# Performance work log

Hardware: AMD Instinct MI355X
Metric: run time of the kernel (lower is better)

## Reference

```python
import jax, jax.numpy as jnp
import numpy as np

B, S, D, H = 8, 2048, 1024, 64  # batch, seq, dimension, attention_head_size


def setup_inputs() -> dict:
    key = jax.random.key(0)
    k0, k1, k2, k3 = jax.random.split(key, 4)
    scale = 1.0 / np.sqrt(D)  # keep activations sane
    return {
        "x": jax.random.normal(k0, (B, S, D), dtype=jnp.float32),
        "Wq": jax.random.normal(k1, (D, H), dtype=jnp.float32) * scale,
        "Wk": jax.random.normal(k2, (D, H), dtype=jnp.float32) * scale,
        "Wv": jax.random.normal(k3, (D, H), dtype=jnp.float32) * scale,
    }


def reference(x, Wq, Wk, Wv):
    # Linear projections (bias=False); W stored as [D, H] == torch weight.T
    q = jnp.einsum("bsd,dh->bsh", x, Wq)
    k = jnp.einsum("bsd,dh->bsh", x, Wk)
    v = jnp.einsum("bsd,dh->bsh", x, Wv)
    # full score matrix, scaled by sqrt(head_size)
    scores = jnp.einsum("bqh,bkh->bqk", q, k) / jnp.sqrt(jnp.float32(H))
    weights = jax.nn.softmax(scores, axis=-1)  # [B, S, S]
    # dropout p=0.0 (eval): identity
    out = jnp.einsum("bqk,bkh->bqh", weights, v)  # [B, S, H]
    return out, weights
```

## Files before the change

### kernel.cpp

```cpp
#include <hip/hip_runtime.h>

#define SB 8
#define SS 2048
#define SD 1024
#define SH 64

typedef float f32x4 __attribute__((ext_vector_type(4)));
typedef __bf16 bf16x8 __attribute__((ext_vector_type(8)));

__device__ __forceinline__ unsigned short f2bf(float f) {
  union { float f; unsigned int u; } v; v.f = f;
  unsigned int u = v.u;
  unsigned int r = u + 0x7FFFu + ((u >> 16) & 1u);
  return (unsigned short)(r >> 16);
}

__global__ void prep_wt(const float* __restrict__ Wq, const float* __restrict__ Wk,
                        const float* __restrict__ Wv, unsigned short* __restrict__ Wt) {
  int idx = blockIdx.x * 256 + threadIdx.x;
  int hc = idx >> 10, d = idx & 1023;
  const float* W = (hc < 64) ? Wq : (hc < 128) ? Wk : Wv;
  int h = hc & 63;
  Wt[idx] = f2bf(W[d * SH + h]);
}

__global__ void __launch_bounds__(512, 2) proj(
    const float* __restrict__ x, const unsigned short* __restrict__ Wt,
    unsigned short* __restrict__ Q, unsigned short* __restrict__ K,
    unsigned short* __restrict__ Vt) {
  __shared__ unsigned short xs[2][32 * 64];
  __shared__ unsigned short Bl[2][192 * 64];

  int tid = threadIdx.x;
  int w = tid >> 6, lane = tid & 63;
  int l15 = lane & 15, kg = lane >> 4;
  int wr = w >> 2, wc = w & 3;
  int m0 = blockIdx.x * 32;

  int srow = tid >> 4, sseg = tid & 15;
  const float* xp = x + (size_t)(m0 + srow) * SD + sseg * 4;
  int swoff = srow * 64 + (((sseg >> 1) ^ (srow & 7)) << 3) + ((sseg & 1) << 2);

#define STAGEB(tt, buf)                                                          \
  {                                                                              \
    _Pragma("unroll") for (int j = 0; j < 3; ++j) {                              \
      int Lb = w * 1024 + j * 8192 + lane * 16;                                  \
      int c = Lb >> 7, cb = Lb & 127;                                            \
      const char* srcp = (const char*)Wt + (size_t)c * 2048 + (tt) * 128 +       \
                         (cb ^ ((c & 7) << 4));                                  \
      __builtin_amdgcn_global_load_lds(                                          \
          (const __attribute__((address_space(1))) unsigned int*)(const void*)srcp, \
          (__attribute__((address_space(3))) unsigned int*)(void*)                \
              ((char*)&Bl[(buf)][0] + w * 1024 + j * 8192),                      \
          16, 0, 0);                                                             \
    }                                                                            \
  }

#define CVTW(RA, buf)                                                           \
  {                                                                             \
    ushort4 cv;                                                                 \
    cv.x = f2bf((RA).x); cv.y = f2bf((RA).y);                                   \
    cv.z = f2bf((RA).z); cv.w = f2bf((RA).w);                                   \
    *(ushort4*)(&xs[(buf)][0] + swoff) = cv;                                    \
  }

  f32x4 acc[3];
#pragma unroll
  for (int nt = 0; nt < 3; ++nt) acc[nt] = f32x4{0.f, 0.f, 0.f, 0.f};

  float4 ra = *(const float4*)xp;
  STAGEB(0, 0);
  CVTW(ra, 0);
  ra = *(const float4*)(xp + 64);
  __syncthreads();

  for (int t = 0; t < 16; ++t) {
    int cur = t & 1, nxt = (t + 1) & 1;
    if (t < 15) CVTW(ra, nxt);
    if (t < 14) ra = *(const float4*)(xp + (t + 2) * 64);
    if (t < 15) STAGEB(t + 1, nxt);

    const char* Bb = (const char*)&Bl[cur][0];
#pragma unroll
    for (int ks = 0; ks < 2; ++ks) {
      int row = wr * 16 + l15;
      int cg = ks * 4 + kg;
      bf16x8 af = *(const bf16x8*)(&xs[cur][0] + row * 64 + ((cg ^ (row & 7)) << 3));
#pragma unroll
      for (int nt = 0; nt < 3; ++nt) {
        int c = wc * 48 + nt * 16 + l15;
        int kb = (ks * 32 + kg * 8) * 2;
        bf16x8 bfr = *(const bf16x8*)(Bb + c * 128 + (kb ^ ((c & 7) << 4)));
        acc[nt] = __builtin_amdgcn_mfma_f32_16x16x32_bf16(af, bfr, acc[nt], 0, 0, 0);
      }
    }
    __syncthreads();
  }

#pragma unroll
  for (int nt = 0; nt < 3; ++nt) {
    int c = wc * 48 + nt * 16 + l15;
    int mat = c >> 6, h = c & 63;
#pragma unroll
    for (int r = 0; r < 4; ++r) {
      int row = m0 + wr * 16 + kg * 4 + r;
      unsigned short bv = f2bf(acc[nt][r]);
      if (mat == 0) {
        Q[(size_t)row * SH + h] = bv;
      } else if (mat == 1) {
        K[(size_t)row * SH + h] = bv;
      } else {
        int bb = row >> 11, key = row & 2047;
        Vt[((size_t)bb * SH + h) * SS + key] = bv;
      }
    }
  }
}

__global__ void __launch_bounds__(512, 4) attn(
    const unsigned short* __restrict__ Q, const unsigned short* __restrict__ Kb,
    const unsigned short* __restrict__ Vt, float* __restrict__ out,
    float* __restrict__ wts) {
  __shared__ float pf[8][16][68];
  __shared__ float mS[8][16], sgS[8][16];

  int b = blockIdx.x & 7, rg = blockIdx.x >> 3;
  int w = threadIdx.x >> 6, lane = threadIdx.x & 63;
  int l15 = lane & 15, kg = lane >> 4;
  int q0 = rg * 16;
  int kv0 = w * 256;

  const unsigned short* Qb  = Q  + (size_t)b * SS * SH;
  const unsigned short* Kbb = Kb + (size_t)b * SS * SH;
  const unsigned short* Vtb = Vt + (size_t)b * SH * SS;

  bf16x8 qf[2];
#pragma unroll
  for (int ks = 0; ks < 2; ++ks)
    qf[ks] = *(const bf16x8*)(Qb + (size_t)(q0 + l15) * SH + ks * 32 + kg * 8);

  f32x4 s[4][4];
#pragma unroll
  for (int kt = 0; kt < 4; ++kt)
#pragma unroll
    for (int n = 0; n < 4; ++n) s[kt][n] = f32x4{0.f, 0.f, 0.f, 0.f};

  for (int kt = 0; kt < 4; ++kt) {
#pragma unroll
    for (int ks = 0; ks < 2; ++ks)
#pragma unroll
      for (int n = 0; n < 4; ++n) {
        bf16x8 kf = *(const bf16x8*)(Kbb + (size_t)(kv0 + kt * 64 + n * 16 + l15) * SH + ks * 32 + kg * 8);
        s[kt][n] = __builtin_amdgcn_mfma_f32_16x16x32_bf16(qf[ks], kf, s[kt][n], 0, 0, 0);
      }
  }

  float m[4], sg[4];
#pragma unroll
  for (int r = 0; r < 4; ++r) {
    float mloc = -1e30f;
#pragma unroll
    for (int kt = 0; kt < 4; ++kt)
#pragma unroll
      for (int n = 0; n < 4; ++n) mloc = fmaxf(mloc, s[kt][n][r]);
    mloc *= 0.125f;
#pragma unroll
    for (int off = 1; off < 16; off <<= 1) mloc = fmaxf(mloc, __shfl_xor(mloc, off));
    float ssum = 0.f;
#pragma unroll
    for (int kt = 0; kt < 4; ++kt)
#pragma unroll
      for (int n = 0; n < 4; ++n) {
        float e = __expf(s[kt][n][r] * 0.125f - mloc);
        s[kt][n][r] = e;
        ssum += e;
      }
#pragma unroll
    for (int off = 1; off < 16; off <<= 1) ssum += __shfl_xor(ssum, off);
    m[r] = mloc; sg[r] = ssum;
  }

  if (l15 == 0) {
#pragma unroll
    for (int r = 0; r < 4; ++r) {
      mS[w][kg * 4 + r] = m[r];
      sgS[w][kg * 4 + r] = sg[r];
    }
  }
  __syncthreads();

  float scal[4];
#pragma unroll
  for (int r = 0; r < 4; ++r) {
    int row = kg * 4 + r;
    float M = -1e30f;
#pragma unroll
    for (int ww = 0; ww < 8; ++ww) M = fmaxf(M, mS[ww][row]);
    float Sg = 0.f;
#pragma unroll
    for (int ww = 0; ww < 8; ++ww) Sg += sgS[ww][row] * __expf(mS[ww][row] - M);
    scal[r] = __expf(m[r] - M) / Sg;
  }

  float* wb = wts + (size_t)b * SS * SS;
  f32x4 oacc[4];
#pragma unroll
  for (int nh = 0; nh < 4; ++nh) oacc[nh] = f32x4{0.f, 0.f, 0.f, 0.f};

  for (int kt = 0; kt < 4; ++kt) {
#pragma unroll
    for (int n = 0; n < 4; ++n)
#pragma unroll
      for (int r = 0; r < 4; ++r)
        pf[w][kg * 4 + r][n * 16 + l15] = s[kt][n][r] * scal[r];
    asm volatile("s_waitcnt lgkmcnt(0)" ::: "memory");

#pragma unroll
    for (int i = 0; i < 4; ++i) {
      int row = i * 4 + kg;
      f32x4 pv4 = *(const f32x4*)&pf[w][row][l15 * 4];
      *(f32x4*)(wb + (size_t)(q0 + row) * SS + kv0 + kt * 64 + l15 * 4) = pv4;
    }

#pragma unroll
    for (int ks = 0; ks < 2; ++ks) {
      f32x4 pa = *(const f32x4*)&pf[w][l15][ks * 32 + kg * 8];
      f32x4 pb = *(const f32x4*)&pf[w][l15][ks * 32 + kg * 8 + 4];
      union { unsigned short us[8]; bf16x8 v; } pu;
#pragma unroll
      for (int i = 0; i < 4; ++i) { pu.us[i] = f2bf(pa[i]); pu.us[4 + i] = f2bf(pb[i]); }
#pragma unroll
      for (int nh = 0; nh < 4; ++nh) {
        bf16x8 vf = *(const bf16x8*)(Vtb + (size_t)(nh * 16 + l15) * SS + kv0 + kt * 64 + ks * 32 + kg * 8);
        oacc[nh] = __builtin_amdgcn_mfma_f32_16x16x32_bf16(pu.v, vf, oacc[nh], 0, 0, 0);
      }
    }
  }

#pragma unroll
  for (int nh = 0; nh < 4; ++nh)
#pragma unroll
    for (int r = 0; r < 4; ++r)
      pf[w][kg * 4 + r][nh * 16 + l15] = oacc[nh][r];
  __syncthreads();

  int tid = threadIdx.x;
#pragma unroll
  for (int half = 0; half < 2; ++half) {
    int e = tid + half * 512;
    int row = e >> 6, col = e & 63;
    float ssum = 0.f;
#pragma unroll
    for (int ww = 0; ww < 8; ++ww) ssum += pf[ww][row][col];
    out[((size_t)b * SS + q0 + row) * SH + col] = ssum;
  }
}

extern "C" void kernel_launch(void* const* d_in, const int* in_sizes, int n_in,
                              void* d_out, int out_size, void* d_ws, size_t ws_size,
                              hipStream_t stream) {
  const float* x  = (const float*)d_in[0];
  const float* Wq = (const float*)d_in[1];
  const float* Wk = (const float*)d_in[2];
  const float* Wv = (const float*)d_in[3];

  unsigned short* Wt = (unsigned short*)d_ws;
  unsigned short* Q  = Wt + 192 * 1024;
  unsigned short* K  = Q + 16384 * 64;
  unsigned short* Vt = K + 16384 * 64;

  float* out = (float*)d_out;
  float* wts = out + (size_t)SB * SS * SH;

  prep_wt<<<768, 256, 0, stream>>>(Wq, Wk, Wv, Wt);
  proj<<<512, 512, 0, stream>>>(x, Wt, Q, K, Vt);
  attn<<<1024, 512, 0, stream>>>(Q, K, Vt, out, wts);
}
```

Before: 93.01 us.

## Split attention into QK-softmax kernel and separate weights-times-V kernel

Removes the P·V product from the attention kernel, which now only computes scores, softmax and writes the weight matrix. A new kernel reads the fp32 weights back from global memory together with transposed V, converts them to bf16 and accumulates the output with MFMA. It uses inline-asm global loads in a three-stage software pipeline. This frees registers and LDS work in the first kernel but adds a full re-read of the large weight matrix and an extra launch.

```diff
diff --git a/kernel.cpp b/kernel.cpp
--- a/kernel.cpp
+++ b/kernel.cpp
@@ -13,6 +13,10 @@
   unsigned int u = v.u;
   unsigned int r = u + 0x7FFFu + ((u >> 16) & 1u);
   return (unsigned short)(r >> 16);
+}
+
+__device__ __forceinline__ bf16x8 asbf(f32x4 x) {
+  union { f32x4 f; bf16x8 b; } u; u.f = x; return u.b;
 }
 
 __global__ void prep_wt(const float* __restrict__ Wq, const float* __restrict__ Wk,
@@ -117,9 +121,8 @@
   }
 }
 
-__global__ void __launch_bounds__(512, 4) attn(
+__global__ void __launch_bounds__(512, 4) qk_sm(
     const unsigned short* __restrict__ Q, const unsigned short* __restrict__ Kb,
-    const unsigned short* __restrict__ Vt, float* __restrict__ out,
     float* __restrict__ wts) {
   __shared__ float pf[8][16][68];
   __shared__ float mS[8][16], sgS[8][16];
@@ -132,7 +135,6 @@
 
   const unsigned short* Qb  = Q  + (size_t)b * SS * SH;
   const unsigned short* Kbb = Kb + (size_t)b * SS * SH;
-  const unsigned short* Vtb = Vt + (size_t)b * SH * SS;
 
   bf16x8 qf[2];
 #pragma unroll
@@ -203,10 +205,6 @@
   }
 
   float* wb = wts + (size_t)b * SS * SS;
-  f32x4 oacc[4];
-#pragma unroll
-  for (int nh = 0; nh < 4; ++nh) oacc[nh] = f32x4{0.f, 0.f, 0.f, 0.f};
-
   for (int kt = 0; kt < 4; ++kt) {
 #pragma unroll
     for (int n = 0; n < 4; ++n)
@@ -221,27 +219,71 @@
       f32x4 pv4 = *(const f32x4*)&pf[w][row][l15 * 4];
       *(f32x4*)(wb + (size_t)(q0 + row) * SS + kv0 + kt * 64 + l15 * 4) = pv4;
     }
-
-#pragma unroll
-    for (int ks = 0; ks < 2; ++ks) {
-      f32x4 pa = *(const f32x4*)&pf[w][l15][ks * 32 + kg * 8];
-      f32x4 pb = *(const f32x4*)&pf[w][l15][ks * 32 + kg * 8 + 4];
-      union { unsigned short us[8]; bf16x8 v; } pu;
-#pragma unroll
-      for (int i = 0; i < 4; ++i) { pu.us[i] = f2bf(pa[i]); pu.us[4 + i] = f2bf(pb[i]); }
-#pragma unroll
-      for (int nh = 0; nh < 4; ++nh) {
-        bf16x8 vf = *(const bf16x8*)(Vtb + (size_t)(nh * 16 + l15) * SS + kv0 + kt * 64 + ks * 32 + kg * 8);
-        oacc[nh] = __builtin_amdgcn_mfma_f32_16x16x32_bf16(pu.v, vf, oacc[nh], 0, 0, 0);
-      }
-    }
-  }
+  }
+}
+
+__global__ void __launch_bounds__(512, 2) wv(
+    const float* __restrict__ wts, const unsigned short* __restrict__ Vt,
+    float* __restrict__ out) {
+  __shared__ float cf[8][16][68];
+
+  int b = blockIdx.x & 7, rg = blockIdx.x >> 3;
+  int w = threadIdx.x >> 6, lane = threadIdx.x & 63;
+  int l15 = lane & 15, kg = lane >> 4;
+  int q0 = rg * 16;
+  int kv0 = w * 256;
+
+  const float* ap = wts + (size_t)b * SS * SS + (size_t)(q0 + l15) * SS + kv0 + kg * 8;
+  const unsigned short* Vtb = Vt + (size_t)b * SH * SS;
+
+  f32x4 rA0_0, rA0_1, rV0_0, rV0_1, rV0_2, rV0_3;
+  f32x4 rA1_0, rA1_1, rV1_0, rV1_1, rV1_2, rV1_3;
+  f32x4 rA2_0, rA2_1, rV2_0, rV2_1, rV2_2, rV2_3;
+
+#define VADDR(KT, NH) (Vtb + (size_t)((NH) * 16 + l15) * SS + kv0 + (KT) * 32 + kg * 8)
+#define GISSUE(S, KT)                                                                     \
+  asm volatile("global_load_dwordx4 %0, %1, off" : "=v"(rA##S##_0) : "v"(ap + (KT) * 32));     \
+  asm volatile("global_load_dwordx4 %0, %1, off" : "=v"(rA##S##_1) : "v"(ap + (KT) * 32 + 4)); \
+  asm volatile("global_load_dwordx4 %0, %1, off" : "=v"(rV##S##_0) : "v"(VADDR(KT, 0)));       \
+  asm volatile("global_load_dwordx4 %0, %1, off" : "=v"(rV##S##_1) : "v"(VADDR(KT, 1)));       \
+  asm volatile("global_load_dwordx4 %0, %1, off" : "=v"(rV##S##_2) : "v"(VADDR(KT, 2)));       \
+  asm volatile("global_load_dwordx4 %0, %1, off" : "=v"(rV##S##_3) : "v"(VADDR(KT, 3)));
+#define GWAIT(N)                            \
+  asm volatile("s_waitcnt vmcnt(" #N ")");  \
+  __builtin_amdgcn_sched_barrier(0);
+#define GCONSUME(S, N)                                                                  \
+  GWAIT(N);                                                                             \
+  {                                                                                     \
+    union { unsigned short us[8]; bf16x8 v; } pu;                                       \
+    _Pragma("unroll") for (int i = 0; i < 4; ++i) {                                     \
+      pu.us[i] = f2bf(rA##S##_0[i]);                                                    \
+      pu.us[4 + i] = f2bf(rA##S##_1[i]);                                                \
+    }                                                                                   \
+    oacc[0] = __builtin_amdgcn_mfma_f32_16x16x32_bf16(pu.v, asbf(rV##S##_0), oacc[0], 0, 0, 0); \
+    oacc[1] = __builtin_amdgcn_mfma_f32_16x16x32_bf16(pu.v, asbf(rV##S##_1), oacc[1], 0, 0, 0); \
+    oacc[2] = __builtin_amdgcn_mfma_f32_16x16x32_bf16(pu.v, asbf(rV##S##_2), oacc[2], 0, 0, 0); \
+    oacc[3] = __builtin_amdgcn_mfma_f32_16x16x32_bf16(pu.v, asbf(rV##S##_3), oacc[3], 0, 0, 0); \
+  }
+
+  f32x4 oacc[4];
+#pragma unroll
+  for (int nh = 0; nh < 4; ++nh) oacc[nh] = f32x4{0.f, 0.f, 0.f, 0.f};
+
+  GISSUE(0, 0); GISSUE(1, 1); GISSUE(2, 2);
+  GCONSUME(0, 12); GISSUE(0, 3);
+  GCONSUME(1, 12); GISSUE(1, 4);
+  GCONSUME(2, 12); GISSUE(2, 5);
+  GCONSUME(0, 12); GISSUE(0, 6);
+  GCONSUME(1, 12); GISSUE(1, 7);
+  GCONSUME(2, 12);
+  GCONSUME(0, 6);
+  GCONSUME(1, 0);
 
 #pragma unroll
   for (int nh = 0; nh < 4; ++nh)
 #pragma unroll
     for (int r = 0; r < 4; ++r)
-      pf[w][kg * 4 + r][nh * 16 + l15] = oacc[nh][r];
+      cf[w][kg * 4 + r][nh * 16 + l15] = oacc[nh][r];
   __syncthreads();
 
   int tid = threadIdx.x;
@@ -251,7 +293,7 @@
     int row = e >> 6, col = e & 63;
     float ssum = 0.f;
 #pragma unroll
-    for (int ww = 0; ww < 8; ++ww) ssum += pf[ww][row][col];
+    for (int ww = 0; ww < 8; ++ww) ssum += cf[ww][row][col];
     out[((size_t)b * SS + q0 + row) * SH + col] = ssum;
   }
 }
@@ -274,5 +316,6 @@
 
   prep_wt<<<768, 256, 0, stream>>>(Wq, Wk, Wv, Wt);
   proj<<<512, 512, 0, stream>>>(x, Wt, Q, K, Vt);
-  attn<<<1024, 512, 0, stream>>>(Q, K, Vt, out, wts);
-}
+  qk_sm<<<1024, 512, 0, stream>>>(Q, K, wts);
+  wv<<<1024, 512, 0, stream>>>(wts, Vt, out);
+}
```

Result: slower. 121.3 us (+30.4%).

## Stage fp32 x tiles via async global-to-LDS loads with deeper A buffering

Applied to the files above, without the earlier changes.

The projection kernel no longer loads x into registers and converts it to bf16 before writing LDS. It now issues direct global_load_lds copies of fp32 x into a 4-deep swizzled LDS ring and converts to bf16 at fragment-read time. Manual waitcnt plus s_barrier replaces __syncthreads so that two A stages stay in flight. The aim is to take register staging and conversion off the load path and overlap memory with MFMA. The cost is four times more LDS for x (32 KB) and repeated per-wave conversion work, which may reduce occupancy.

```diff
diff --git a/kernel.cpp b/kernel.cpp
--- a/kernel.cpp
+++ b/kernel.cpp
@@ -28,7 +28,7 @@
     const float* __restrict__ x, const unsigned short* __restrict__ Wt,
     unsigned short* __restrict__ Q, unsigned short* __restrict__ K,
     unsigned short* __restrict__ Vt) {
-  __shared__ unsigned short xs[2][32 * 64];
+  __shared__ float xs_f[4][32 * 64];
   __shared__ unsigned short Bl[2][192 * 64];
 
   int tid = threadIdx.x;
@@ -37,9 +37,21 @@
   int wr = w >> 2, wc = w & 3;
   int m0 = blockIdx.x * 32;
 
-  int srow = tid >> 4, sseg = tid & 15;
-  const float* xp = x + (size_t)(m0 + srow) * SD + sseg * 4;
-  int swoff = srow * 64 + (((sseg >> 1) ^ (srow & 7)) << 3) + ((sseg & 1) << 2);
+  int arow = ((w * 64 + lane) >> 4);
+  int acol = (lane & 15) * 4;
+  int agrp = acol >> 3, awithin = acol & 7;
+  const float* asrc = x + (size_t)(m0 + arow) * SD +
+                      (((agrp ^ (arow & 7)) << 3) + awithin);
+
+#define STAGEA(tt, buf)                                                          \
+  {                                                                              \
+    __builtin_amdgcn_global_load_lds(                                            \
+        (const __attribute__((address_space(1))) unsigned int*)(const void*)     \
+            (asrc + (tt) * 64),                                                  \
+        (__attribute__((address_space(3))) unsigned int*)(void*)                 \
+            ((char*)&xs_f[(buf)][0] + w * 1024),                                 \
+        16, 0, 0);                                                               \
+  }
 
 #define STAGEB(tt, buf)                                                          \
   {                                                                              \
@@ -56,45 +68,51 @@
     }                                                                            \
   }
 
-#define CVTW(RA, buf)                                                           \
-  {                                                                             \
-    ushort4 cv;                                                                 \
-    cv.x = f2bf((RA).x); cv.y = f2bf((RA).y);                                   \
-    cv.z = f2bf((RA).z); cv.w = f2bf((RA).w);                                   \
-    *(ushort4*)(&xs[(buf)][0] + swoff) = cv;                                    \
-  }
-
   f32x4 acc[3];
 #pragma unroll
   for (int nt = 0; nt < 3; ++nt) acc[nt] = f32x4{0.f, 0.f, 0.f, 0.f};
 
-  float4 ra = *(const float4*)xp;
+  STAGEA(0, 0);
   STAGEB(0, 0);
-  CVTW(ra, 0);
-  ra = *(const float4*)(xp + 64);
-  __syncthreads();
+  STAGEA(1, 1);
+  asm volatile("s_waitcnt vmcnt(1) lgkmcnt(0)" ::: "memory");
+  __builtin_amdgcn_sched_barrier(0);
+  __builtin_amdgcn_s_barrier();
+  __builtin_amdgcn_sched_barrier(0);
 
   for (int t = 0; t < 16; ++t) {
-    int cur = t & 1, nxt = (t + 1) & 1;
-    if (t < 15) CVTW(ra, nxt);
-    if (t < 14) ra = *(const float4*)(xp + (t + 2) * 64);
-    if (t < 15) STAGEB(t + 1, nxt);
-
-    const char* Bb = (const char*)&Bl[cur][0];
+    int abuf = t & 3, bbuf = t & 1;
+    if (t < 15) STAGEB(t + 1, (t + 1) & 1);
+    if (t < 14) STAGEA(t + 2, (t + 2) & 3);
+
+    const char* Bb = (const char*)&Bl[bbuf][0];
 #pragma unroll
     for (int ks = 0; ks < 2; ++ks) {
       int row = wr * 16 + l15;
       int cg = ks * 4 + kg;
-      bf16x8 af = *(const bf16x8*)(&xs[cur][0] + row * 64 + ((cg ^ (row & 7)) << 3));
+      const float* ap = &xs_f[abuf][row * 64 + ((cg ^ (row & 7)) << 3)];
+      f32x4 a0 = *(const f32x4*)ap;
+      f32x4 a1 = *(const f32x4*)(ap + 4);
+      union { unsigned short us[8]; bf16x8 v; } cvu;
+#pragma unroll
+      for (int i = 0; i < 4; ++i) { cvu.us[i] = f2bf(a0[i]); cvu.us[4 + i] = f2bf(a1[i]); }
 #pragma unroll
       for (int nt = 0; nt < 3; ++nt) {
         int c = wc * 48 + nt * 16 + l15;
         int kb = (ks * 32 + kg * 8) * 2;
         bf16x8 bfr = *(const bf16x8*)(Bb + c * 128 + (kb ^ ((c & 7) << 4)));
-        acc[nt] = __builtin_amdgcn_mfma_f32_16x16x32_bf16(af, bfr, acc[nt], 0, 0, 0);
-      }
-    }
-    __syncthreads();
+        acc[nt] = __builtin_amdgcn_mfma_f32_16x16x32_bf16(cvu.v, bfr, acc[nt], 0, 0, 0);
+      }
+    }
+
+    if (t < 14) {
+      asm volatile("s_waitcnt vmcnt(1) lgkmcnt(0)" ::: "memory");
+    } else {
+      asm volatile("s_waitcnt vmcnt(0) lgkmcnt(0)" ::: "memory");
+    }
+    __builtin_amdgcn_sched_barrier(0);
+    __builtin_amdgcn_s_barrier();
+    __builtin_amdgcn_sched_barrier(0);
   }
 
 #pragma unroll
```

Result: slower. 95.24 us (+2.4%).

## Use 1024-thread attention blocks covering 32 query rows each

Applied to the files above, without the earlier changes.

Changes the attention kernel to launch 512 blocks of 1024 threads, where each block handles 32 query rows split across two row-halves of eight waves each, using dynamic shared memory. The intent is fewer, larger blocks that share scheduling and reduction overhead. In exchange, barriers now synchronize sixteen waves, an extra barrier is added before the output reduction, and the LDS per block roughly doubles, which may limit occupancy. Launch bounds of 1024x8 may also force register limits.

```diff
diff --git a/kernel.cpp b/kernel.cpp
--- a/kernel.cpp
+++ b/kernel.cpp
@@ -117,18 +117,22 @@
   }
 }
 
-__global__ void __launch_bounds__(512, 4) attn(
+__global__ void __launch_bounds__(1024, 8) attn(
     const unsigned short* __restrict__ Q, const unsigned short* __restrict__ Kb,
     const unsigned short* __restrict__ Vt, float* __restrict__ out,
     float* __restrict__ wts) {
-  __shared__ float pf[8][16][68];
-  __shared__ float mS[8][16], sgS[8][16];
+  extern __shared__ __align__(16) float dyn[];
+  float (*pf)[16][68] = (float (*)[16][68])dyn;
+  float* mS  = dyn + 16 * 16 * 68;
+  float* sgS = mS + 256;
 
   int b = blockIdx.x & 7, rg = blockIdx.x >> 3;
-  int w = threadIdx.x >> 6, lane = threadIdx.x & 63;
+  int tid = threadIdx.x;
+  int w = tid >> 6, lane = tid & 63;
   int l15 = lane & 15, kg = lane >> 4;
-  int q0 = rg * 16;
-  int kv0 = w * 256;
+  int rh = w & 1, ws = w >> 1;
+  int q0 = rg * 32 + rh * 16;
+  int kv0 = ws * 256;
 
   const unsigned short* Qb  = Q  + (size_t)b * SS * SH;
   const unsigned short* Kbb = Kb + (size_t)b * SS * SH;
@@ -183,8 +187,8 @@
   if (l15 == 0) {
 #pragma unroll
     for (int r = 0; r < 4; ++r) {
-      mS[w][kg * 4 + r] = m[r];
-      sgS[w][kg * 4 + r] = sg[r];
+      mS[w * 16 + kg * 4 + r] = m[r];
+      sgS[w * 16 + kg * 4 + r] = sg[r];
     }
   }
   __syncthreads();
@@ -195,10 +199,13 @@
     int row = kg * 4 + r;
     float M = -1e30f;
 #pragma unroll
-    for (int ww = 0; ww < 8; ++ww) M = fmaxf(M, mS[ww][row]);
+    for (int j = 0; j < 8; ++j) M = fmaxf(M, mS[(rh + 2 * j) * 16 + row]);
     float Sg = 0.f;
 #pragma unroll
-    for (int ww = 0; ww < 8; ++ww) Sg += sgS[ww][row] * __expf(mS[ww][row] - M);
+    for (int j = 0; j < 8; ++j) {
+      int ww = rh + 2 * j;
+      Sg += sgS[ww * 16 + row] * __expf(mS[ww * 16 + row] - M);
+    }
     scal[r] = __expf(m[r] - M) / Sg;
   }
 
@@ -237,6 +244,7 @@
     }
   }
 
+  __syncthreads();
 #pragma unroll
   for (int nh = 0; nh < 4; ++nh)
 #pragma unroll
@@ -244,15 +252,15 @@
       pf[w][kg * 4 + r][nh * 16 + l15] = oacc[nh][r];
   __syncthreads();
 
-  int tid = threadIdx.x;
 #pragma unroll
   for (int half = 0; half < 2; ++half) {
-    int e = tid + half * 512;
+    int e = tid + half * 1024;
     int row = e >> 6, col = e & 63;
+    int rhe = row >> 4, lr = row & 15;
     float ssum = 0.f;
 #pragma unroll
-    for (int ww = 0; ww < 8; ++ww) ssum += pf[ww][row][col];
-    out[((size_t)b * SS + q0 + row) * SH + col] = ssum;
+    for (int j = 0; j < 8; ++j) ssum += pf[rhe + 2 * j][lr][col];
+    out[((size_t)b * SS + rg * 32 + row) * SH + col] = ssum;
   }
 }
 
@@ -272,7 +280,9 @@
   float* out = (float*)d_out;
   float* wts = out + (size_t)SB * SS * SH;
 
+  size_t attn_lds = (size_t)(16 * 16 * 68 + 256 + 256) * sizeof(float);
+
   prep_wt<<<768, 256, 0, stream>>>(Wq, Wk, Wv, Wt);
   proj<<<512, 512, 0, stream>>>(x, Wt, Q, K, Vt);
-  attn<<<1024, 512, 0, stream>>>(Q, K, Vt, out, wts);
-}
+  attn<<<512, 1024, attn_lds, stream>>>(Q, K, Vt, out, wts);
+}
```

After: 225.8 us. 143% more time.
